# Kernel optimization log

Hardware: AMD Instinct MI355X
Metric: run time of the kernel (lower is better)

Reference implementation:

```python
import jax, jax.numpy as jnp
import numpy as np

N = 1024      # number of residues/tokens
D = 768       # node feature dim (heads * d_head)
H = 12        # heads
DH = D // H   # d_head = 64
DP = 128      # pair feature dim
SCALE = 0.125 # 1/sqrt(d_head)
EPS = 1e-5

def _ln(x, w, b):
    m = jnp.mean(x, axis=-1, keepdims=True)
    v = jnp.var(x, axis=-1, keepdims=True)
    return (x - m) * jax.lax.rsqrt(v + EPS) * w + b

def setup_inputs() -> dict:
    key = jax.random.key(0)
    ks = jax.random.split(key, 8)
    s = 0.02
    return {
        "node_feats": jax.random.normal(ks[0], (N, D), dtype=jnp.float32),
        "pair_feats": jax.random.normal(ks[1], (N, N, DP), dtype=jnp.float32),
        "ln_node_w": jnp.ones((D,), jnp.float32), "ln_node_b": jnp.zeros((D,), jnp.float32),
        "pair_ln_w": jnp.ones((DP,), jnp.float32), "pair_ln_b": jnp.zeros((DP,), jnp.float32),
        "qkv_W": jax.random.normal(ks[2], (D, 3 * D), dtype=jnp.float32) * s,
        "qkv_b": jnp.zeros((3 * D,), jnp.float32),
        "q_ln_w": jnp.ones((D,), jnp.float32), "q_ln_b": jnp.zeros((D,), jnp.float32),
        "k_ln_w": jnp.ones((D,), jnp.float32), "k_ln_b": jnp.zeros((D,), jnp.float32),
        "g_W": jax.random.normal(ks[3], (D, D), dtype=jnp.float32) * s,
        "g_b": jnp.zeros((D,), jnp.float32),
        "bias_W": jax.random.normal(ks[4], (DP, H), dtype=jnp.float32) * s,
        "bias_b": jnp.zeros((H,), jnp.float32),
        "out_W": jax.random.normal(ks[5], (D, D), dtype=jnp.float32) * s,
        "out_b": jnp.zeros((D,), jnp.float32),
        "mask": jax.random.bernoulli(ks[6], 0.9, (N, N)),
    }

def reference(node_feats, pair_feats, ln_node_w, ln_node_b, pair_ln_w, pair_ln_b,
              qkv_W, qkv_b, q_ln_w, q_ln_b, k_ln_w, k_ln_b,
              g_W, g_b, bias_W, bias_b, out_W, out_b, mask):
    x = _ln(node_feats, ln_node_w, ln_node_b)                 # [N, D]
    p = _ln(pair_feats, pair_ln_w, pair_ln_b)                 # [N, N, DP]
    q, k, v = jnp.split(x @ qkv_W + qkv_b, 3, axis=-1)        # each [N, D]
    q = _ln(q, q_ln_w, q_ln_b)
    k = _ln(k, k_ln_w, k_ln_b)
    g = x @ g_W + g_b                                         # [N, D]
    bias = jnp.einsum('ijp,ph->hij', p, bias_W) + bias_b[:, None, None]  # [H, N, N]
    bias = bias + jnp.where(mask[None, :, :], 0.0, -10000.0)
    q = q.reshape(N, H, DH); k = k.reshape(N, H, DH); v = v.reshape(N, H, DH)
    logits = jnp.einsum('ihd,jhd->hij', q, k) * SCALE + bias  # [H, N, N]
    attn = jax.nn.softmax(logits, axis=-1)
    out = jnp.einsum('hij,jhd->ihd', attn, v).reshape(N, D)   # [N, D]
    out = jax.nn.sigmoid(g) * out
    return out @ out_W + out_b
```

## Files before the change

kernel.cpp:

```cpp
#include <hip/hip_runtime.h>
#include <math.h>

#define N_TOK 1024
#define D_DIM 768
#define H_N   12
#define DH    64
#define DP    128
#define SCALE 0.125f
#define EPS   1e-5f
#define NN    (N_TOK * N_TOK)

__global__ __launch_bounds__(128) void prep_kernel(
    const float* __restrict__ pair_ln_w, const float* __restrict__ pair_ln_b,
    const float* __restrict__ bias_W, const float* __restrict__ bias_b,
    float* __restrict__ W2, float* __restrict__ S2cb)
{
    __shared__ float Ws[DP * H_N];
    __shared__ float slw[DP], slb[DP];
    int t = threadIdx.x;
    slw[t] = pair_ln_w[t];
    slb[t] = pair_ln_b[t];
    for (int idx = t; idx < DP * H_N; idx += 128) Ws[idx] = bias_W[idx];
    __syncthreads();
    for (int idx = t; idx < DP * H_N; idx += 128) {
        int c = idx / H_N;
        W2[idx] = slw[c] * Ws[idx];
    }
    if (t < 24) {
        int h = t % H_N;
        bool isS = t < H_N;
        float s = 0.f;
        for (int c = 0; c < DP; ++c)
            s += (isS ? slw[c] : slb[c]) * Ws[c * H_N + h];
        S2cb[t] = isS ? s : (s + bias_b[h]);
    }
}

__global__ __launch_bounds__(256) void ln_kernel(
    const float* __restrict__ in, float* __restrict__ out,
    int istride, int ostride,
    const float* __restrict__ w, const float* __restrict__ b)
{
    int row = blockIdx.x;
    int tid = threadIdx.x;
    const float* ip = in + (size_t)row * istride;
    float v0 = ip[tid], v1 = ip[tid + 256], v2 = ip[tid + 512];
    float s = v0 + v1 + v2;
    float q = v0 * v0 + v1 * v1 + v2 * v2;
    __shared__ float red[8];
    #pragma unroll
    for (int o = 32; o > 0; o >>= 1) {
        s += __shfl_down(s, o);
        q += __shfl_down(q, o);
    }
    int lane = tid & 63, wv = tid >> 6;
    if (lane == 0) { red[wv] = s; red[4 + wv] = q; }
    __syncthreads();
    if (tid == 0) {
        float ss = red[0] + red[1] + red[2] + red[3];
        float qq = red[4] + red[5] + red[6] + red[7];
        float mean = ss * (1.f / 768.f);
        float var = qq * (1.f / 768.f) - mean * mean;
        red[0] = mean;
        red[1] = rsqrtf(var + EPS);
    }
    __syncthreads();
    float mean = red[0], rstd = red[1];
    float* op = out + (size_t)row * ostride;
    op[tid]       = (v0 - mean) * rstd * w[tid]       + b[tid];
    op[tid + 256] = (v1 - mean) * rstd * w[tid + 256] + b[tid + 256];
    op[tid + 512] = (v2 - mean) * rstd * w[tid + 512] + b[tid + 512];
}

__global__ __launch_bounds__(256) void sgemm(
    const float* __restrict__ A, int lda,
    const float* __restrict__ B0, int ldb0, const float* __restrict__ bias0,
    const float* __restrict__ B1, int ldb1, const float* __restrict__ bias1,
    int split, float* __restrict__ C, int ldc, int K)
{
    __shared__ __align__(16) float As[16 * 68];
    __shared__ __align__(16) float Bs[16 * 132];
    int tid = threadIdx.x;
    int tx = tid & 15, ty = tid >> 4;
    int m0 = blockIdx.y * 64, n0 = blockIdx.x * 128;
    const float* Bp; const float* bp; int ldb, bcol0;
    if (n0 < split) { Bp = B0; bp = bias0; ldb = ldb0; bcol0 = n0; }
    else            { Bp = B1; bp = bias1; ldb = ldb1; bcol0 = n0 - split; }

    float acc[4][8] = {};
    int ar = tid >> 2, ak = (tid & 3) * 4;
    int bk = tid >> 5, bc = (tid & 31) * 4;

    for (int kt = 0; kt < K; kt += 16) {
        float4 av  = *(const float4*)&A[(size_t)(m0 + ar) * lda + kt + ak];
        float4 b0v = *(const float4*)&Bp[(size_t)(kt + bk) * ldb + bcol0 + bc];
        float4 b1v = *(const float4*)&Bp[(size_t)(kt + bk + 8) * ldb + bcol0 + bc];
        As[(ak + 0) * 68 + ar] = av.x;
        As[(ak + 1) * 68 + ar] = av.y;
        As[(ak + 2) * 68 + ar] = av.z;
        As[(ak + 3) * 68 + ar] = av.w;
        *(float4*)&Bs[bk * 132 + bc] = b0v;
        *(float4*)&Bs[(bk + 8) * 132 + bc] = b1v;
        __syncthreads();
        #pragma unroll
        for (int kk = 0; kk < 16; ++kk) {
            float4 a  = *(const float4*)&As[kk * 68 + ty * 4];
            float4 b0 = *(const float4*)&Bs[kk * 132 + tx * 4];
            float4 b1 = *(const float4*)&Bs[kk * 132 + 64 + tx * 4];
            float av_[4] = { a.x, a.y, a.z, a.w };
            float bv_[8] = { b0.x, b0.y, b0.z, b0.w, b1.x, b1.y, b1.z, b1.w };
            #pragma unroll
            for (int u = 0; u < 4; ++u)
                #pragma unroll
                for (int i = 0; i < 8; ++i)
                    acc[u][i] += av_[u] * bv_[i];
        }
        __syncthreads();
    }
    float4 bb0 = *(const float4*)&bp[bcol0 + tx * 4];
    float4 bb1 = *(const float4*)&bp[bcol0 + 64 + tx * 4];
    #pragma unroll
    for (int u = 0; u < 4; ++u) {
        float* cp = &C[(size_t)(m0 + ty * 4 + u) * ldc + n0];
        float4 o0, o1;
        o0.x = acc[u][0] + bb0.x; o0.y = acc[u][1] + bb0.y;
        o0.z = acc[u][2] + bb0.z; o0.w = acc[u][3] + bb0.w;
        o1.x = acc[u][4] + bb1.x; o1.y = acc[u][5] + bb1.y;
        o1.z = acc[u][6] + bb1.z; o1.w = acc[u][7] + bb1.w;
        *(float4*)&cp[tx * 4]      = o0;
        *(float4*)&cp[64 + tx * 4] = o1;
    }
}

__global__ __launch_bounds__(256) void bias_kernel(
    const float* __restrict__ pair, const int* __restrict__ mask,
    const float* __restrict__ W2, const float* __restrict__ S2cb,
    float* __restrict__ biasbuf)
{
    __shared__ __align__(16) float sW2[DP * H_N];
    __shared__ float sS[H_N], sC[H_N];
    int tid = threadIdx.x;
    for (int t = tid; t < DP * H_N; t += 256) sW2[t] = W2[t];
    if (tid < H_N) { sS[tid] = S2cb[tid]; sC[tid] = S2cb[H_N + tid]; }
    __syncthreads();

    int gid = blockIdx.x * 256 + tid;
    const float4* p4 = (const float4*)(pair + (size_t)gid * DP);
    float sum = 0.f, ssq = 0.f;
    float dot[H_N];
    #pragma unroll
    for (int h = 0; h < H_N; ++h) dot[h] = 0.f;

    #pragma unroll 4
    for (int c4 = 0; c4 < 32; ++c4) {
        float4 v = p4[c4];
        float e[4] = { v.x, v.y, v.z, v.w };
        #pragma unroll
        for (int k = 0; k < 4; ++k) {
            float x = e[k];
            sum += x; ssq += x * x;
            const float4* wp4 = (const float4*)&sW2[(c4 * 4 + k) * H_N];
            float4 w0 = wp4[0], w1 = wp4[1], w2 = wp4[2];
            dot[0] += x * w0.x; dot[1] += x * w0.y; dot[2]  += x * w0.z; dot[3]  += x * w0.w;
            dot[4] += x * w1.x; dot[5] += x * w1.y; dot[6]  += x * w1.z; dot[7]  += x * w1.w;
            dot[8] += x * w2.x; dot[9] += x * w2.y; dot[10] += x * w2.z; dot[11] += x * w2.w;
        }
    }
    float mean = sum * (1.f / 128.f);
    float var  = ssq * (1.f / 128.f) - mean * mean;
    float rstd = rsqrtf(var + EPS);
    float mz = (mask[gid] != 0) ? 0.f : -10000.f;
    #pragma unroll
    for (int h = 0; h < H_N; ++h)
        biasbuf[(size_t)h * NN + gid] = (dot[h] - mean * sS[h]) * rstd + sC[h] + mz;
}

__global__ __launch_bounds__(256) void attn_kernel(
    const float* __restrict__ xw, const float* __restrict__ biasbuf,
    float* __restrict__ attn_out)
{
    const int h  = blockIdx.y;
    const int i0 = blockIdx.x * 16;
    const int tid = threadIdx.x;
    const int tx = tid & 15, ty = tid >> 4;

    __shared__ __align__(16) float Qs[16 * 68];
    __shared__ __align__(16) float Ks[32 * 64];
    __shared__ __align__(16) float Vs[32 * 68];
    __shared__ float Ps[16 * 33];

    {
        int r = tid >> 4, c4 = tid & 15;
        float4 v = *(const float4*)(xw + (size_t)(i0 + r) * 3072 + h * 64 + c4 * 4);
        float* d = &Qs[r * 68 + c4 * 4];
        d[0] = v.x * SCALE; d[1] = v.y * SCALE; d[2] = v.z * SCALE; d[3] = v.w * SCALE;
    }

    float m = -1e30f, l = 0.f;
    float a0 = 0.f, a1 = 0.f, a2 = 0.f, a3 = 0.f;
    const float* brow = biasbuf + (size_t)h * NN + (size_t)(i0 + ty) * N_TOK;
    const int swz = tx & 7;
    const float* qrow = &Qs[ty * 68];
    const float* k0p = &Ks[(2 * tx) << 6];
    const float* k1p = &Ks[((2 * tx) << 6) + 64];

    for (int j0 = 0; j0 < N_TOK; j0 += 32) {
        #pragma unroll
        for (int q2 = 0; q2 < 2; ++q2) {
            int idx = tid + q2 * 256;
            int r = idx >> 4, c4 = idx & 15;
            const float* gp = xw + (size_t)(j0 + r) * 3072 + 768 + h * 64 + c4 * 4;
            float4 kv = *(const float4*)gp;
            *(float4*)&Ks[(r << 6) + ((c4 ^ ((r >> 1) & 7)) << 2)] = kv;
            float4 vv = *(const float4*)(gp + 768);
            *(float4*)&Vs[r * 68 + c4 * 4] = vv;
        }
        __syncthreads();

        float s0a = 0.f, s0b = 0.f, s1a = 0.f, s1b = 0.f;
        #pragma unroll
        for (int d4 = 0; d4 < 16; ++d4) {
            float4 q  = *(const float4*)&qrow[d4 << 2];
            int o = (d4 ^ swz) << 2;
            float4 ka = *(const float4*)&k0p[o];
            float4 kb = *(const float4*)&k1p[o];
            s0a += q.x * ka.x + q.y * ka.y;
            s0b += q.z * ka.z + q.w * ka.w;
            s1a += q.x * kb.x + q.y * kb.y;
            s1b += q.z * kb.z + q.w * kb.w;
        }
        float2 bb = *(const float2*)&brow[j0 + 2 * tx];
        float s0 = s0a + s0b + bb.x;
        float s1 = s1a + s1b + bb.y;

        float mt = fmaxf(s0, s1);
        #pragma unroll
        for (int o = 1; o < 16; o <<= 1) mt = fmaxf(mt, __shfl_xor(mt, o));
        float mn = fmaxf(m, mt);
        float al = __expf(m - mn);
        float p0 = __expf(s0 - mn);
        float p1 = __expf(s1 - mn);
        float rs = p0 + p1;
        #pragma unroll
        for (int o = 1; o < 16; o <<= 1) rs += __shfl_xor(rs, o);
        l = l * al + rs;
        m = mn;
        a0 *= al; a1 *= al; a2 *= al; a3 *= al;
        Ps[ty * 33 + 2 * tx]     = p0;
        Ps[ty * 33 + 2 * tx + 1] = p1;
        __syncthreads();

        const float* prow = &Ps[ty * 33];
        #pragma unroll
        for (int j = 0; j < 32; ++j) {
            float pv = prow[j];
            float4 vv = *(const float4*)&Vs[j * 68 + tx * 4];
            a0 += pv * vv.x; a1 += pv * vv.y; a2 += pv * vv.z; a3 += pv * vv.w;
        }
        __syncthreads();
    }

    float inv = 1.f / l;
    int row = i0 + ty;
    float4 gv = *(const float4*)(xw + (size_t)row * 3072 + 2304 + h * 64 + tx * 4);
    float* op = attn_out + (size_t)row * 768 + h * 64 + tx * 4;
    op[0] = a0 * inv / (1.f + __expf(-gv.x));
    op[1] = a1 * inv / (1.f + __expf(-gv.y));
    op[2] = a2 * inv / (1.f + __expf(-gv.z));
    op[3] = a3 * inv / (1.f + __expf(-gv.w));
}

extern "C" void kernel_launch(void* const* d_in, const int* in_sizes, int n_in,
                              void* d_out, int out_size, void* d_ws, size_t ws_size,
                              hipStream_t stream)
{
    const float* node      = (const float*)d_in[0];
    const float* pair      = (const float*)d_in[1];
    const float* ln_node_w = (const float*)d_in[2];
    const float* ln_node_b = (const float*)d_in[3];
    const float* pair_ln_w = (const float*)d_in[4];
    const float* pair_ln_b = (const float*)d_in[5];
    const float* qkv_W     = (const float*)d_in[6];
    const float* qkv_b     = (const float*)d_in[7];
    const float* q_ln_w    = (const float*)d_in[8];
    const float* q_ln_b    = (const float*)d_in[9];
    const float* k_ln_w    = (const float*)d_in[10];
    const float* k_ln_b    = (const float*)d_in[11];
    const float* g_W       = (const float*)d_in[12];
    const float* g_b       = (const float*)d_in[13];
    const float* bias_W    = (const float*)d_in[14];
    const float* bias_b    = (const float*)d_in[15];
    const float* out_W     = (const float*)d_in[16];
    const float* out_b     = (const float*)d_in[17];
    const int*   mask      = (const int*)d_in[18];
    float* out = (float*)d_out;

    float* ws      = (float*)d_ws;
    float* x       = ws;
    float* xw      = x + 786432;
    float* W2      = xw + 3145728;
    float* S2cb    = W2 + 1536;
    float* biasbuf = S2cb + 32;
    float* attn_o  = biasbuf + 12582912;

    prep_kernel<<<1, 128, 0, stream>>>(pair_ln_w, pair_ln_b, bias_W, bias_b, W2, S2cb);
    ln_kernel<<<1024, 256, 0, stream>>>(node, x, 768, 768, ln_node_w, ln_node_b);
    sgemm<<<dim3(24, 16), 256, 0, stream>>>(x, 768,
                                            qkv_W, 2304, qkv_b,
                                            g_W, 768, g_b,
                                            2304, xw, 3072, 768);
    ln_kernel<<<1024, 256, 0, stream>>>(xw, xw, 3072, 3072, q_ln_w, q_ln_b);
    ln_kernel<<<1024, 256, 0, stream>>>(xw + 768, xw + 768, 3072, 3072, k_ln_w, k_ln_b);
    bias_kernel<<<4096, 256, 0, stream>>>(pair, mask, W2, S2cb, biasbuf);
    attn_kernel<<<dim3(64, 12), 256, 0, stream>>>(xw, biasbuf, attn_o);
    sgemm<<<dim3(6, 16), 256, 0, stream>>>(attn_o, 768,
                                           out_W, 768, out_b,
                                           out_W, 768, out_b,
                                           1 << 30, out, 768, 768);
}
```

Measured before the change: 1.094 ms.

## Stage pair rows via LDS for coalesced bias loads; widen attention key tile

The bias kernel now loads 64 pair rows per step cooperatively into swizzled shared memory so global reads are coalesced, instead of each thread streaming its own 512-byte row. Four threads then split each row's channels and combine their partial sums with shuffles. The attention kernel doubles the key tile to 64 and gives each thread a 2x2 query-key block for QK, which improves register reuse. It also shares the per-row rescale factors and final normalisers through shared memory. The cost is more LDS use, which may lower occupancy, plus extra shuffle reductions.

```diff
diff --git a/kernel.cpp b/kernel.cpp
--- a/kernel.cpp
+++ b/kernel.cpp
@@ -137,42 +137,65 @@
     const float* __restrict__ W2, const float* __restrict__ S2cb,
     float* __restrict__ biasbuf)
 {
+    __shared__ __align__(16) float4 Lp[64 * 32];
     __shared__ __align__(16) float sW2[DP * H_N];
     __shared__ float sS[H_N], sC[H_N];
     int tid = threadIdx.x;
     for (int t = tid; t < DP * H_N; t += 256) sW2[t] = W2[t];
     if (tid < H_N) { sS[tid] = S2cb[tid]; sC[tid] = S2cb[H_N + tid]; }
-    __syncthreads();
-
-    int gid = blockIdx.x * 256 + tid;
-    const float4* p4 = (const float4*)(pair + (size_t)gid * DP);
-    float sum = 0.f, ssq = 0.f;
-    float dot[H_N];
-    #pragma unroll
-    for (int h = 0; h < H_N; ++h) dot[h] = 0.f;
-
-    #pragma unroll 4
-    for (int c4 = 0; c4 < 32; ++c4) {
-        float4 v = p4[c4];
-        float e[4] = { v.x, v.y, v.z, v.w };
-        #pragma unroll
-        for (int k = 0; k < 4; ++k) {
-            float x = e[k];
-            sum += x; ssq += x * x;
-            const float4* wp4 = (const float4*)&sW2[(c4 * 4 + k) * H_N];
-            float4 w0 = wp4[0], w1 = wp4[1], w2 = wp4[2];
-            dot[0] += x * w0.x; dot[1] += x * w0.y; dot[2]  += x * w0.z; dot[3]  += x * w0.w;
-            dot[4] += x * w1.x; dot[5] += x * w1.y; dot[6]  += x * w1.z; dot[7]  += x * w1.w;
-            dot[8] += x * w2.x; dot[9] += x * w2.y; dot[10] += x * w2.z; dot[11] += x * w2.w;
-        }
-    }
-    float mean = sum * (1.f / 128.f);
-    float var  = ssq * (1.f / 128.f) - mean * mean;
-    float rstd = rsqrtf(var + EPS);
-    float mz = (mask[gid] != 0) ? 0.f : -10000.f;
-    #pragma unroll
-    for (int h = 0; h < H_N; ++h)
-        biasbuf[(size_t)h * NN + gid] = (dot[h] - mean * sS[h]) * rstd + sC[h] + mz;
+
+    int r = tid >> 2, qq = tid & 3;
+    const float4* pair4 = (const float4*)pair;
+
+    for (int c = 0; c < 4; ++c) {
+        int gid0 = (blockIdx.x * 4 + c) * 64;
+        __syncthreads();
+        #pragma unroll
+        for (int i = 0; i < 8; ++i) {
+            int n = i * 256 + tid;
+            int row = n >> 5, c4 = n & 31;
+            Lp[row * 32 + ((c4 + 2 * row) & 31)] = pair4[(size_t)gid0 * 32 + n];
+        }
+        __syncthreads();
+
+        float sum = 0.f, ssq = 0.f;
+        float dot[H_N];
+        #pragma unroll
+        for (int h = 0; h < H_N; ++h) dot[h] = 0.f;
+
+        #pragma unroll
+        for (int i = 0; i < 8; ++i) {
+            int c4 = qq + 4 * i;
+            float4 v = Lp[r * 32 + ((c4 + 2 * r) & 31)];
+            float e[4] = { v.x, v.y, v.z, v.w };
+            #pragma unroll
+            for (int k = 0; k < 4; ++k) {
+                float x = e[k];
+                sum += x; ssq += x * x;
+                const float4* wp4 = (const float4*)&sW2[(c4 * 4 + k) * H_N];
+                float4 w0 = wp4[0], w1 = wp4[1], w2 = wp4[2];
+                dot[0] += x * w0.x; dot[1] += x * w0.y; dot[2]  += x * w0.z; dot[3]  += x * w0.w;
+                dot[4] += x * w1.x; dot[5] += x * w1.y; dot[6]  += x * w1.z; dot[7]  += x * w1.w;
+                dot[8] += x * w2.x; dot[9] += x * w2.y; dot[10] += x * w2.z; dot[11] += x * w2.w;
+            }
+        }
+        #pragma unroll
+        for (int o = 1; o < 4; o <<= 1) {
+            sum += __shfl_xor(sum, o);
+            ssq += __shfl_xor(ssq, o);
+            #pragma unroll
+            for (int h = 0; h < H_N; ++h) dot[h] += __shfl_xor(dot[h], o);
+        }
+        float mean = sum * (1.f / 128.f);
+        float var  = ssq * (1.f / 128.f) - mean * mean;
+        float rstd = rsqrtf(var + EPS);
+        float mz = (mask[gid0 + r] != 0) ? 0.f : -10000.f;
+        #pragma unroll
+        for (int s = 0; s < 3; ++s) {
+            int h = qq * 3 + s;
+            biasbuf[(size_t)h * NN + gid0 + r] = (dot[h] - mean * sS[h]) * rstd + sC[h] + mz;
+        }
+    }
 }
 
 __global__ __launch_bounds__(256) void attn_kernel(
@@ -182,12 +205,12 @@
     const int h  = blockIdx.y;
     const int i0 = blockIdx.x * 16;
     const int tid = threadIdx.x;
-    const int tx = tid & 15, ty = tid >> 4;
 
     __shared__ __align__(16) float Qs[16 * 68];
-    __shared__ __align__(16) float Ks[32 * 64];
-    __shared__ __align__(16) float Vs[32 * 68];
-    __shared__ float Ps[16 * 33];
+    __shared__ __align__(16) float Ks[64 * 64];
+    __shared__ __align__(16) float Vs[64 * 68];
+    __shared__ float Ps[16 * 68];
+    __shared__ float alrow[16], lfin[16];
 
     {
         int r = tid >> 4, c4 = tid & 15;
@@ -196,63 +219,80 @@
         d[0] = v.x * SCALE; d[1] = v.y * SCALE; d[2] = v.z * SCALE; d[3] = v.w * SCALE;
     }
 
-    float m = -1e30f, l = 0.f;
+    const int tj = tid & 31, tq = tid >> 5;
+    const float* q0p = &Qs[(2 * tq) * 68];
+    const float* q1p = q0p + 68;
+    const float* k0p = &Ks[(2 * tj) << 6];
+    const float* k1p = k0p + 64;
+    const int swz = tj & 7;
+    const float* brow0 = biasbuf + (size_t)h * NN + (size_t)(i0 + 2 * tq) * N_TOK;
+    const float* brow1 = brow0 + N_TOK;
+    const int tx = tid & 15, ty = tid >> 4;
+
+    float m0r = -1e30f, m1r = -1e30f, l0 = 0.f, l1 = 0.f;
     float a0 = 0.f, a1 = 0.f, a2 = 0.f, a3 = 0.f;
-    const float* brow = biasbuf + (size_t)h * NN + (size_t)(i0 + ty) * N_TOK;
-    const int swz = tx & 7;
-    const float* qrow = &Qs[ty * 68];
-    const float* k0p = &Ks[(2 * tx) << 6];
-    const float* k1p = &Ks[((2 * tx) << 6) + 64];
-
-    for (int j0 = 0; j0 < N_TOK; j0 += 32) {
-        #pragma unroll
-        for (int q2 = 0; q2 < 2; ++q2) {
-            int idx = tid + q2 * 256;
-            int r = idx >> 4, c4 = idx & 15;
-            const float* gp = xw + (size_t)(j0 + r) * 3072 + 768 + h * 64 + c4 * 4;
+
+    for (int j0 = 0; j0 < N_TOK; j0 += 64) {
+        #pragma unroll
+        for (int q2 = 0; q2 < 4; ++q2) {
+            int idx = q2 * 256 + tid;
+            int rr = idx >> 4, c4 = idx & 15;
+            const float* gp = xw + (size_t)(j0 + rr) * 3072 + 768 + h * 64 + c4 * 4;
             float4 kv = *(const float4*)gp;
-            *(float4*)&Ks[(r << 6) + ((c4 ^ ((r >> 1) & 7)) << 2)] = kv;
+            *(float4*)&Ks[(rr << 6) + ((c4 ^ ((rr >> 1) & 7)) << 2)] = kv;
             float4 vv = *(const float4*)(gp + 768);
-            *(float4*)&Vs[r * 68 + c4 * 4] = vv;
-        }
-        __syncthreads();
-
-        float s0a = 0.f, s0b = 0.f, s1a = 0.f, s1b = 0.f;
+            *(float4*)&Vs[rr * 68 + c4 * 4] = vv;
+        }
+        __syncthreads();
+
+        float4 s00 = {0,0,0,0}, s01 = {0,0,0,0}, s10 = {0,0,0,0}, s11 = {0,0,0,0};
         #pragma unroll
         for (int d4 = 0; d4 < 16; ++d4) {
-            float4 q  = *(const float4*)&qrow[d4 << 2];
+            float4 qa = *(const float4*)&q0p[d4 << 2];
+            float4 qb = *(const float4*)&q1p[d4 << 2];
             int o = (d4 ^ swz) << 2;
             float4 ka = *(const float4*)&k0p[o];
             float4 kb = *(const float4*)&k1p[o];
-            s0a += q.x * ka.x + q.y * ka.y;
-            s0b += q.z * ka.z + q.w * ka.w;
-            s1a += q.x * kb.x + q.y * kb.y;
-            s1b += q.z * kb.z + q.w * kb.w;
-        }
-        float2 bb = *(const float2*)&brow[j0 + 2 * tx];
-        float s0 = s0a + s0b + bb.x;
-        float s1 = s1a + s1b + bb.y;
-
-        float mt = fmaxf(s0, s1);
-        #pragma unroll
-        for (int o = 1; o < 16; o <<= 1) mt = fmaxf(mt, __shfl_xor(mt, o));
-        float mn = fmaxf(m, mt);
-        float al = __expf(m - mn);
-        float p0 = __expf(s0 - mn);
-        float p1 = __expf(s1 - mn);
-        float rs = p0 + p1;
-        #pragma unroll
-        for (int o = 1; o < 16; o <<= 1) rs += __shfl_xor(rs, o);
-        l = l * al + rs;
-        m = mn;
-        a0 *= al; a1 *= al; a2 *= al; a3 *= al;
-        Ps[ty * 33 + 2 * tx]     = p0;
-        Ps[ty * 33 + 2 * tx + 1] = p1;
-        __syncthreads();
-
-        const float* prow = &Ps[ty * 33];
-        #pragma unroll
-        for (int j = 0; j < 32; ++j) {
+            s00.x += qa.x * ka.x; s00.y += qa.y * ka.y; s00.z += qa.z * ka.z; s00.w += qa.w * ka.w;
+            s01.x += qa.x * kb.x; s01.y += qa.y * kb.y; s01.z += qa.z * kb.z; s01.w += qa.w * kb.w;
+            s10.x += qb.x * ka.x; s10.y += qb.y * ka.y; s10.z += qb.z * ka.z; s10.w += qb.w * ka.w;
+            s11.x += qb.x * kb.x; s11.y += qb.y * kb.y; s11.z += qb.z * kb.z; s11.w += qb.w * kb.w;
+        }
+        float2 b0 = *(const float2*)&brow0[j0 + 2 * tj];
+        float2 b1 = *(const float2*)&brow1[j0 + 2 * tj];
+        float S00 = s00.x + s00.y + s00.z + s00.w + b0.x;
+        float S01 = s01.x + s01.y + s01.z + s01.w + b0.y;
+        float S10 = s10.x + s10.y + s10.z + s10.w + b1.x;
+        float S11 = s11.x + s11.y + s11.z + s11.w + b1.y;
+
+        float mt0 = fmaxf(S00, S01), mt1 = fmaxf(S10, S11);
+        #pragma unroll
+        for (int o = 1; o < 32; o <<= 1) {
+            mt0 = fmaxf(mt0, __shfl_xor(mt0, o));
+            mt1 = fmaxf(mt1, __shfl_xor(mt1, o));
+        }
+        float mn0 = fmaxf(m0r, mt0), mn1 = fmaxf(m1r, mt1);
+        float al0 = __expf(m0r - mn0), al1 = __expf(m1r - mn1);
+        float p00 = __expf(S00 - mn0), p01 = __expf(S01 - mn0);
+        float p10 = __expf(S10 - mn1), p11 = __expf(S11 - mn1);
+        float rs0 = p00 + p01, rs1 = p10 + p11;
+        #pragma unroll
+        for (int o = 1; o < 32; o <<= 1) {
+            rs0 += __shfl_xor(rs0, o);
+            rs1 += __shfl_xor(rs1, o);
+        }
+        l0 = l0 * al0 + rs0; l1 = l1 * al1 + rs1;
+        m0r = mn0; m1r = mn1;
+        *(float2*)&Ps[(2 * tq) * 68 + 2 * tj]     = make_float2(p00, p01);
+        *(float2*)&Ps[(2 * tq + 1) * 68 + 2 * tj] = make_float2(p10, p11);
+        if (tj == 0) { alrow[2 * tq] = al0; alrow[2 * tq + 1] = al1; }
+        __syncthreads();
+
+        float als = alrow[ty];
+        a0 *= als; a1 *= als; a2 *= als; a3 *= als;
+        const float* prow = &Ps[ty * 68];
+        #pragma unroll
+        for (int j = 0; j < 64; ++j) {
             float pv = prow[j];
             float4 vv = *(const float4*)&Vs[j * 68 + tx * 4];
             a0 += pv * vv.x; a1 += pv * vv.y; a2 += pv * vv.z; a3 += pv * vv.w;
@@ -260,7 +300,10 @@
         __syncthreads();
     }
 
-    float inv = 1.f / l;
+    if (tj == 0) { lfin[2 * tq] = l0; lfin[2 * tq + 1] = l1; }
+    __syncthreads();
+
+    float inv = 1.f / lfin[ty];
     int row = i0 + ty;
     float4 gv = *(const float4*)(xw + (size_t)row * 3072 + 2304 + h * 64 + tx * 4);
     float* op = attn_out + (size_t)row * 768 + h * 64 + tx * 4;
```

Measured after the change: 1.033 ms. 5.6% less time.
